# Optimization experiments

Measured on AMD Instinct MI355X. Metric: run time of the kernel, lower is better.

The kernel has to match this reference:

```python
import jax, jax.numpy as jnp
import numpy as np

D_MODEL = 2048
N_EXPERTS = 64
TOP_K = 2


def setup_inputs() -> dict:
    key = jax.random.key(0)
    kx, kw, kb = jax.random.split(key, 3)
    x = jax.random.normal(kx, (4, 8192, D_MODEL), dtype=jnp.float32)
    # nn.Linear(input_size, n_experts): weight [n_experts, input_size], bias [n_experts]
    W = jax.random.normal(kw, (N_EXPERTS, D_MODEL), dtype=jnp.float32) * (1.0 / np.sqrt(D_MODEL))
    b = jax.random.normal(kb, (N_EXPERTS,), dtype=jnp.float32) * 0.01
    return {"x": x, "W": W, "b": b}


def reference(x, W, b):
    B, S, D = x.shape
    # logits over experts: [B, S, E]
    logits = jnp.einsum("bsd,ed->bse", x, W) + b
    probs = jax.nn.softmax(logits, axis=-1)
    # top-k along experts (sorted descending, matching torch.topk)
    top_w, top_idx = jax.lax.top_k(probs, TOP_K)
    return top_idx, top_w
```

## Files before the change

kernel.cpp:

```cpp
#include <hip/hip_runtime.h>
#include <stdint.h>

#define D_MODEL 2048
#define N_EXP   64
#define TOKS    16
#define WAVES   4
#define KW      (D_MODEL / WAVES)
#define KSS     32
#define NSS     (KW / KSS)
#define ROW_F4  8
#define BUF_F4  (TOKS * ROW_F4)

__global__ void make_Wq2(const float* __restrict__ W, float* __restrict__ Wq2) {
    int o  = blockIdx.x * 256 + threadIdx.x;
    int i  = o & 3;
    int eg = (o >> 2) & 15;
    int j  = (o >> 6) & 3;
    int kq = o >> 8;
    Wq2[o] = W[(16 * j + eg) * D_MODEL + 4 * kq + i];
}

union SMemU {
    float4 xs[2 * WAVES * BUF_F4];
    float  red[2][TOKS * 65];
};

__global__ __launch_bounds__(256, 8)
void router_d(const float* __restrict__ x, const float4* __restrict__ Wq2,
              const float* __restrict__ bias, float* __restrict__ out, int n_tokens)
{
    __shared__ SMemU sm;
    const int tid  = threadIdx.x;
    const int lane = tid & 63;
    const int wv   = tid >> 6;
    const int tg   = lane >> 4;
    const int eg   = lane & 15;
    const int tok0 = blockIdx.x * TOKS;
    const int kw   = wv * KW;

    const int trow = lane >> 3;
    const int c    = lane & 7;
    const int gc   = c ^ (trow & 3);

    float acc[4][4];
    #pragma unroll
    for (int tt = 0; tt < 4; ++tt)
        #pragma unroll
        for (int j = 0; j < 4; ++j) acc[tt][j] = 0.f;

    float4* b0 = sm.xs + (0 * WAVES + wv) * BUF_F4;
    float4* b1 = sm.xs + (1 * WAVES + wv) * BUF_F4;

    auto stage = [&](int s, float4* lb) {
        const int kb = kw + s * KSS;
        #pragma unroll
        for (int it = 0; it < 2; ++it) {
            const int t = 8 * it + trow;
            const float* gp = x + (size_t)(tok0 + t) * D_MODEL + kb + 4 * gc;
            __builtin_amdgcn_global_load_lds(
                (const __attribute__((address_space(1))) void*)gp,
                (__attribute__((address_space(3))) void*)(lb + it * 64), 16, 0, 0);
        }
    };

    stage(0, b0);

    for (int s = 0; s < NSS; ++s) {
        float4* cb = (s & 1) ? b1 : b0;
        if (s + 1 < NSS) {
            stage(s + 1, (s & 1) ? b0 : b1);
            asm volatile("s_waitcnt vmcnt(2)" ::: "memory");
        } else {
            asm volatile("s_waitcnt vmcnt(0)" ::: "memory");
        }
        const int kb = kw + s * KSS;
        #pragma unroll
        for (int q = 0; q < KSS / 4; ++q) {
            const int kq = (kb >> 2) + q;
            float4 xv[4];
            #pragma unroll
            for (int tt = 0; tt < 4; ++tt) {
                const int t = 4 * tt + tg;
                xv[tt] = cb[(size_t)t * ROW_F4 + (q ^ tg)];
            }
            const float4* wp = Wq2 + (size_t)kq * 64 + eg;
            #pragma unroll
            for (int j = 0; j < 4; ++j) {
                const float4 w4 = wp[16 * j];
                #pragma unroll
                for (int tt = 0; tt < 4; ++tt) {
                    acc[tt][j] = fmaf(w4.x, xv[tt].x, acc[tt][j]);
                    acc[tt][j] = fmaf(w4.y, xv[tt].y, acc[tt][j]);
                    acc[tt][j] = fmaf(w4.z, xv[tt].z, acc[tt][j]);
                    acc[tt][j] = fmaf(w4.w, xv[tt].w, acc[tt][j]);
                }
            }
        }
    }

    __syncthreads();
    if (wv >= 2) {
        float* R = sm.red[wv - 2];
        #pragma unroll
        for (int tt = 0; tt < 4; ++tt)
            #pragma unroll
            for (int j = 0; j < 4; ++j)
                R[(4 * tt + tg) * 65 + 16 * j + eg] = acc[tt][j];
    }
    __syncthreads();
    if (wv < 2) {
        const float* R = sm.red[wv];
        #pragma unroll
        for (int tt = 0; tt < 4; ++tt)
            #pragma unroll
            for (int j = 0; j < 4; ++j)
                acc[tt][j] += R[(4 * tt + tg) * 65 + 16 * j + eg];
    }
    __syncthreads();
    if (wv == 1) {
        float* R = sm.red[0];
        #pragma unroll
        for (int tt = 0; tt < 4; ++tt)
            #pragma unroll
            for (int j = 0; j < 4; ++j)
                R[(4 * tt + tg) * 65 + 16 * j + eg] = acc[tt][j];
    }
    __syncthreads();

    if (wv == 0) {
        const float* R = sm.red[0];
        float bj[4];
        #pragma unroll
        for (int j = 0; j < 4; ++j) bj[j] = bias[16 * j + eg];
        float* ow = out + 2 * (size_t)n_tokens;

        #pragma unroll
        for (int tt = 0; tt < 4; ++tt) {
            float v[4];
            #pragma unroll
            for (int j = 0; j < 4; ++j)
                v[j] = acc[tt][j] + R[(4 * tt + tg) * 65 + 16 * j + eg] + bj[j];
            float v1 = v[0]; int i1 = eg;
            float v2 = -3.4e38f; int i2 = 1 << 20;
            #pragma unroll
            for (int j = 1; j < 4; ++j) {
                const int e = 16 * j + eg;
                if (v[j] > v1)      { v2 = v1; i2 = i1; v1 = v[j]; i1 = e; }
                else if (v[j] > v2) { v2 = v[j]; i2 = e; }
            }
            #pragma unroll
            for (int m = 1; m < 16; m <<= 1) {
                float b1 = __shfl_xor(v1, m, 64); int j1 = __shfl_xor(i1, m, 64);
                float b2 = __shfl_xor(v2, m, 64); int j2 = __shfl_xor(i2, m, 64);
                bool aw = (v1 > b1) || (v1 == b1 && i1 < j1);
                float lw_v = aw ? b1 : v1;  int lw_i = aw ? j1 : i1;
                float ws_v = aw ? v2 : b2;  int ws_i = aw ? i2 : j2;
                float nv1  = aw ? v1 : b1;  int ni1  = aw ? i1 : j1;
                bool sw = (lw_v > ws_v) || (lw_v == ws_v && lw_i < ws_i);
                v1 = nv1;               i1 = ni1;
                v2 = sw ? lw_v : ws_v;  i2 = sw ? lw_i : ws_i;
            }
            float ssum = 0.f;
            #pragma unroll
            for (int j = 0; j < 4; ++j) ssum += __expf(v[j] - v1);
            #pragma unroll
            for (int m = 1; m < 16; m <<= 1) ssum += __shfl_xor(ssum, m, 64);
            const float inv = 1.0f / ssum;
            const float w1  = inv;
            const float w2  = __expf(v2 - v1) * inv;

            if (eg == tt) {
                const int g = tok0 + 4 * tt + tg;
                float2 fi; fi.x = (float)i1; fi.y = (float)i2;
                ((float2*)out)[g] = fi;
                float2 fw; fw.x = w1; fw.y = w2;
                ((float2*)ow)[g] = fw;
            }
        }
    }
}

extern "C" void kernel_launch(void* const* d_in, const int* in_sizes, int n_in,
                              void* d_out, int out_size, void* d_ws, size_t ws_size,
                              hipStream_t stream) {
    const float* x = (const float*)d_in[0];
    const float* W = (const float*)d_in[1];
    const float* b = (const float*)d_in[2];
    float* out = (float*)d_out;
    float* Wq2 = (float*)d_ws;
    const int n_tokens = in_sizes[0] / D_MODEL;

    make_Wq2<<<(D_MODEL * N_EXP) / 256, 256, 0, stream>>>(W, Wq2);
    router_d<<<n_tokens / TOKS, 256, 0, stream>>>(x, (const float4*)Wq2, b, out, n_tokens);
}
```

Measured before the change: 503.7 us.

## Replace LDS double-buffered x staging with direct global float4 loads

Removes the async global-to-LDS double-buffer pipeline for x tiles and instead has each lane load its four token rows straight from global memory as float4 in an unrolled loop. Launch bounds drop from 8 to 4 blocks per SM, which gives more registers per thread. The intent is to cut LDS traffic, waitcnt stalls and swizzle overhead. The cost is that x reads become strided across lanes: each 16-lane group reads the same address, so coalescing relies on broadcast and cache, and there may be less latency hiding.

```diff
diff --git a/kernel.cpp b/kernel.cpp
--- a/kernel.cpp
+++ b/kernel.cpp
@@ -6,10 +6,7 @@
 #define TOKS    16
 #define WAVES   4
 #define KW      (D_MODEL / WAVES)
-#define KSS     32
-#define NSS     (KW / KSS)
-#define ROW_F4  8
-#define BUF_F4  (TOKS * ROW_F4)
+#define KQW     (KW / 4)
 
 __global__ void make_Wq2(const float* __restrict__ W, float* __restrict__ Wq2) {
     int o  = blockIdx.x * 256 + threadIdx.x;
@@ -20,27 +17,18 @@
     Wq2[o] = W[(16 * j + eg) * D_MODEL + 4 * kq + i];
 }
 
-union SMemU {
-    float4 xs[2 * WAVES * BUF_F4];
-    float  red[2][TOKS * 65];
-};
-
-__global__ __launch_bounds__(256, 8)
+__global__ __launch_bounds__(256, 4)
 void router_d(const float* __restrict__ x, const float4* __restrict__ Wq2,
               const float* __restrict__ bias, float* __restrict__ out, int n_tokens)
 {
-    __shared__ SMemU sm;
+    __shared__ float red[2][TOKS * 65];
     const int tid  = threadIdx.x;
     const int lane = tid & 63;
     const int wv   = tid >> 6;
     const int tg   = lane >> 4;
     const int eg   = lane & 15;
     const int tok0 = blockIdx.x * TOKS;
-    const int kw   = wv * KW;
-
-    const int trow = lane >> 3;
-    const int c    = lane & 7;
-    const int gc   = c ^ (trow & 3);
+    const int kq0  = wv * KQW;
 
     float acc[4][4];
     #pragma unroll
@@ -48,59 +36,34 @@
         #pragma unroll
         for (int j = 0; j < 4; ++j) acc[tt][j] = 0.f;
 
-    float4* b0 = sm.xs + (0 * WAVES + wv) * BUF_F4;
-    float4* b1 = sm.xs + (1 * WAVES + wv) * BUF_F4;
+    const float4* xr[4];
+    #pragma unroll
+    for (int tt = 0; tt < 4; ++tt)
+        xr[tt] = (const float4*)(x + (size_t)(tok0 + 4 * tt + tg) * D_MODEL);
 
-    auto stage = [&](int s, float4* lb) {
-        const int kb = kw + s * KSS;
+    #pragma unroll 4
+    for (int q = 0; q < KQW; ++q) {
+        const int kq = kq0 + q;
+        float4 xv[4];
         #pragma unroll
-        for (int it = 0; it < 2; ++it) {
-            const int t = 8 * it + trow;
-            const float* gp = x + (size_t)(tok0 + t) * D_MODEL + kb + 4 * gc;
-            __builtin_amdgcn_global_load_lds(
-                (const __attribute__((address_space(1))) void*)gp,
-                (__attribute__((address_space(3))) void*)(lb + it * 64), 16, 0, 0);
-        }
-    };
-
-    stage(0, b0);
-
-    for (int s = 0; s < NSS; ++s) {
-        float4* cb = (s & 1) ? b1 : b0;
-        if (s + 1 < NSS) {
-            stage(s + 1, (s & 1) ? b0 : b1);
-            asm volatile("s_waitcnt vmcnt(2)" ::: "memory");
-        } else {
-            asm volatile("s_waitcnt vmcnt(0)" ::: "memory");
-        }
-        const int kb = kw + s * KSS;
+        for (int tt = 0; tt < 4; ++tt) xv[tt] = xr[tt][kq];
+        const float4* wp = Wq2 + (size_t)kq * 64 + eg;
         #pragma unroll
-        for (int q = 0; q < KSS / 4; ++q) {
-            const int kq = (kb >> 2) + q;
-            float4 xv[4];
+        for (int j = 0; j < 4; ++j) {
+            const float4 w4 = wp[16 * j];
             #pragma unroll
             for (int tt = 0; tt < 4; ++tt) {
-                const int t = 4 * tt + tg;
-                xv[tt] = cb[(size_t)t * ROW_F4 + (q ^ tg)];
-            }
-            const float4* wp = Wq2 + (size_t)kq * 64 + eg;
-            #pragma unroll
-            for (int j = 0; j < 4; ++j) {
-                const float4 w4 = wp[16 * j];
-                #pragma unroll
-                for (int tt = 0; tt < 4; ++tt) {
-                    acc[tt][j] = fmaf(w4.x, xv[tt].x, acc[tt][j]);
-                    acc[tt][j] = fmaf(w4.y, xv[tt].y, acc[tt][j]);
-                    acc[tt][j] = fmaf(w4.z, xv[tt].z, acc[tt][j]);
-                    acc[tt][j] = fmaf(w4.w, xv[tt].w, acc[tt][j]);
-                }
+                acc[tt][j] = fmaf(w4.x, xv[tt].x, acc[tt][j]);
+                acc[tt][j] = fmaf(w4.y, xv[tt].y, acc[tt][j]);
+                acc[tt][j] = fmaf(w4.z, xv[tt].z, acc[tt][j]);
+                acc[tt][j] = fmaf(w4.w, xv[tt].w, acc[tt][j]);
             }
         }
     }
 
     __syncthreads();
     if (wv >= 2) {
-        float* R = sm.red[wv - 2];
+        float* R = red[wv - 2];
         #pragma unroll
         for (int tt = 0; tt < 4; ++tt)
             #pragma unroll
@@ -109,7 +72,7 @@
     }
     __syncthreads();
     if (wv < 2) {
-        const float* R = sm.red[wv];
+        const float* R = red[wv];
         #pragma unroll
         for (int tt = 0; tt < 4; ++tt)
             #pragma unroll
@@ -118,7 +81,7 @@
     }
     __syncthreads();
     if (wv == 1) {
-        float* R = sm.red[0];
+        float* R = red[0];
         #pragma unroll
         for (int tt = 0; tt < 4; ++tt)
             #pragma unroll
@@ -128,7 +91,7 @@
     __syncthreads();
 
     if (wv == 0) {
-        const float* R = sm.red[0];
+        const float* R = red[0];
         float bj[4];
         #pragma unroll
         for (int j = 0; j < 4; ++j) bj[j] = bias[16 * j + eg];
```

New measurement: 570.8 us. 13.3% more time.
